# Kernel tuning notes

Measured on AMD Instinct MI355X. Metric: run time of the kernel, lower is better.

## Reference

```python
import jax, jax.numpy as jnp
import numpy as np

MAX_K_QK = 32
MAX_K_V = 32
MAX_K_KNOW = 64
N_HEADS = 12
EPS = 1e-8
LN_EPS = 1e-6


def layer_norm(x, scale, bias):
    mean = jnp.mean(x, axis=-1, keepdims=True)
    var = jnp.mean(jnp.square(x - mean), axis=-1, keepdims=True)
    return (x - mean) / jnp.sqrt(var + LN_EPS) * scale + bias


def threshold_gate(scores, tau, max_k):
    raw = scores - tau
    gate = jnp.where(raw > 0, raw, 1e-8 * jnp.exp(raw))
    exp_gate = jnp.exp(gate) - 1.0
    k = min(max_k, scores.shape[-1])
    topk_vals, _ = jax.lax.top_k(exp_gate, k)
    thr = topk_vals[:, :, -1:]
    exp_gate = jnp.where(exp_gate >= thr, exp_gate, 0.0)
    gate_sum = exp_gate.sum(axis=-1, keepdims=True) + EPS
    gate_strength = jnp.tanh(exp_gate.max(axis=-1, keepdims=True))
    return exp_gate / gate_sum * gate_strength


@jax.checkpoint
def sense_emit_sparse(x, emb, w, gate, idx):
    # x:[B,S,D] emb/w:[N,D] gate/idx:[B,S,k] -> [B,S,D]
    sel_emb = emb[idx]
    sel_w = w[idx]
    act = jnp.einsum('bsd,bskd->bsk', x, sel_emb) * gate
    return jnp.einsum('bsk,bskd->bsd', act, sel_w)


def _forward(x, qk_emb, qk_w, v_emb, v_w, know_emb, know_w, neuron_emb,
             proj_attn_k, proj_attn_b, proj_know_k, proj_know_b,
             tau_attn_k, tau_attn_b, tau_know_k, tau_know_b,
             expand_O, ln1_scale, ln1_bias, ln2_scale, ln2_bias):
    B, S, D = x.shape
    n_qk = qk_emb.shape[0]
    n_v = v_emb.shape[0]
    n_know = know_emb.shape[0]
    emb_norm = neuron_emb / (jnp.linalg.norm(neuron_emb, axis=-1, keepdims=True) + EPS)
    qk_low = emb_norm[:n_qk]
    v_low = emb_norm[n_qk:n_qk + n_v]
    know_low = emb_norm[n_qk + n_v:]

    # ---- attention circuit (deterministic: dropout = identity) ----
    xn = layer_norm(x, ln1_scale, ln1_bias)
    h_all = xn @ proj_attn_k + proj_attn_b
    h_Q, h_K, h_V = jnp.split(h_all, 3, axis=-1)
    tau_all = xn @ tau_attn_k + tau_attn_b
    g_Q = threshold_gate(h_Q @ qk_low.T, tau_all[:, :, 0:1], MAX_K_QK)
    g_K = threshold_gate(h_K @ qk_low.T, tau_all[:, :, 1:2], MAX_K_QK)
    g_V = threshold_gate(h_V @ v_low.T, tau_all[:, :, 2:3], MAX_K_V)
    tk_g_Q, tk_i_Q = jax.lax.top_k(g_Q, MAX_K_QK)
    tk_g_K, tk_i_K = jax.lax.top_k(g_K, MAX_K_QK)
    tk_g_V, tk_i_V = jax.lax.top_k(g_V, MAX_K_V)
    Q = sense_emit_sparse(xn, qk_emb, qk_w, tk_g_Q, tk_i_Q)
    K = sense_emit_sparse(xn, qk_emb, qk_w, tk_g_K, tk_i_K)
    V = sense_emit_sparse(xn, v_emb, v_w, tk_g_V, tk_i_V)
    d_head = D // N_HEADS
    Q = Q.reshape(B, S, N_HEADS, d_head).transpose(0, 2, 1, 3)
    K = K.reshape(B, S, N_HEADS, d_head).transpose(0, 2, 1, 3)
    V = V.reshape(B, S, N_HEADS, d_head).transpose(0, 2, 1, 3)
    scores = jnp.einsum('bhsd,bhtd->bhst', Q, K) / jnp.sqrt(jnp.float32(d_head))
    causal = jnp.tril(jnp.ones((S, S), dtype=jnp.bool_))
    scores = jnp.where(causal, scores, jnp.finfo(scores.dtype).min)
    attn_w = jax.nn.softmax(scores, axis=-1)
    attn_out = jnp.einsum('bhst,bhtd->bhsd', attn_w, V)
    attn_out = attn_out.transpose(0, 2, 1, 3).reshape(B, S, D) @ expand_O
    t_qk, t_v = 1.0 / n_qk, 1.0 / n_v
    a_aux = (((g_Q.mean(axis=(0, 1)) - t_qk) ** 2).sum() * n_qk
             + ((g_K.mean(axis=(0, 1)) - t_qk) ** 2).sum() * n_qk
             + ((g_V.mean(axis=(0, 1)) - t_v) ** 2).sum() * n_v)
    x = x + attn_out

    # ---- knowledge circuit ----
    xn = layer_norm(x, ln2_scale, ln2_bias)
    h = xn @ proj_know_k + proj_know_b
    tau = xn @ tau_know_k + tau_know_b
    gate = threshold_gate(h @ know_low.T, tau, MAX_K_KNOW)
    tk_gate, tk_idx = jax.lax.top_k(gate, MAX_K_KNOW)
    know_out = sense_emit_sparse(xn, know_emb, know_w, tk_gate, tk_idx)
    t_k = 1.0 / n_know
    k_aux = ((gate.mean(axis=(0, 1)) - t_k) ** 2).sum() * n_know
    x = x + know_out
    return x, a_aux + k_aux


def _unit_norm(key, shape):
    v = jax.random.normal(key, shape, jnp.float32)
    return v / (jnp.linalg.norm(v, axis=-1, keepdims=True) + 1e-8)


def setup_inputs() -> dict:
    key = jax.random.key(0)
    ks = jax.random.split(key, 16)
    B, S, D = 4, 1024, 768
    d_space, n_qk, n_v, n_know = 128, 1024, 1024, 4096
    return {
        'x': jax.random.normal(ks[0], (B, S, D), jnp.float32),
        'qk_emb': _unit_norm(ks[1], (n_qk, D)),
        'qk_w': _unit_norm(ks[2], (n_qk, D)),
        'v_emb': _unit_norm(ks[3], (n_v, D)),
        'v_w': _unit_norm(ks[4], (n_v, D)),
        'know_emb': _unit_norm(ks[5], (n_know, D)),
        'know_w': _unit_norm(ks[6], (n_know, D)),
        'neuron_emb': jax.random.normal(ks[7], (n_qk + n_v + n_know, d_space), jnp.float32) * 0.02,
        'proj_attn_k': jax.random.normal(ks[8], (D, 3 * d_space), jnp.float32) * 0.02,
        'proj_attn_b': jnp.zeros((3 * d_space,), jnp.float32),
        'proj_know_k': jax.random.normal(ks[9], (D, d_space), jnp.float32) * 0.02,
        'proj_know_b': jnp.zeros((d_space,), jnp.float32),
        'tau_attn_k': jax.random.normal(ks[10], (D, 3), jnp.float32) * 0.02,
        'tau_attn_b': jnp.zeros((3,), jnp.float32),
        'tau_know_k': jax.random.normal(ks[11], (D, 1), jnp.float32) * 0.02,
        'tau_know_b': jnp.zeros((1,), jnp.float32),
        'expand_O': jax.random.normal(ks[12], (D, D), jnp.float32) * 0.02,
        'ln1_scale': jnp.ones((D,), jnp.float32),
        'ln1_bias': jnp.zeros((D,), jnp.float32),
        'ln2_scale': jnp.ones((D,), jnp.float32),
        'ln2_bias': jnp.zeros((D,), jnp.float32),
    }


def reference(x, qk_emb, qk_w, v_emb, v_w, know_emb, know_w, neuron_emb,
              proj_attn_k, proj_attn_b, proj_know_k, proj_know_b,
              tau_attn_k, tau_attn_b, tau_know_k, tau_know_b,
              expand_O, ln1_scale, ln1_bias, ln2_scale, ln2_bias):
    return _forward(x, qk_emb, qk_w, v_emb, v_w, know_emb, know_w, neuron_emb,
                    proj_attn_k, proj_attn_b, proj_know_k, proj_know_b,
                    tau_attn_k, tau_attn_b, tau_know_k, tau_know_b,
                    expand_O, ln1_scale, ln1_bias, ln2_scale, ln2_bias)
```

## Files before the change

kernel.cpp:

```cpp
#include <hip/hip_runtime.h>
#include <math.h>

#define TOK 4096

#define O_EMBN   0
#define O_XN     786432
#define O_HALL   3932160
#define O_TAU    5505024
#define O_TAUK   5517312
#define O_GVQ    5521408
#define O_GVK    5652480
#define O_GVV    5783552
#define O_GIQ    5914624
#define O_GIK    6045696
#define O_GIV    6176768
#define O_QB     6307840
#define O_KB     9453568
#define O_VB     12599296
#define O_SUM    15745024

__global__ void k_zero(float* p, int n){
  int i = blockIdx.x*blockDim.x + threadIdx.x;
  if (i < n) p[i] = 0.f;
}

__global__ void k_normemb(const float* __restrict__ e, float* __restrict__ o){
  int row = blockIdx.x; int t = threadIdx.x;
  float v = e[(size_t)row*128 + t];
  __shared__ float red[128];
  red[t] = v*v; __syncthreads();
  for (int s=64; s>0; s>>=1){ if (t<s) red[t]+=red[t+s]; __syncthreads(); }
  float norm = sqrtf(red[0]) + 1e-8f;
  o[(size_t)row*128 + t] = v / norm;
}

__global__ void k_ln(const float* __restrict__ x, const float* __restrict__ sc,
                     const float* __restrict__ bi, float* __restrict__ o){
  int tok = blockIdx.x; int t = threadIdx.x;
  __shared__ float red[256];
  const float* xr = x + (size_t)tok*768;
  float a0=xr[t], a1=xr[t+256], a2=xr[t+512];
  red[t] = a0+a1+a2; __syncthreads();
  for (int s=128; s>0; s>>=1){ if (t<s) red[t]+=red[t+s]; __syncthreads(); }
  float mean = red[0] * (1.f/768.f);
  __syncthreads();
  float d0=a0-mean, d1=a1-mean, d2=a2-mean;
  red[t] = d0*d0+d1*d1+d2*d2; __syncthreads();
  for (int s=128; s>0; s>>=1){ if (t<s) red[t]+=red[t+s]; __syncthreads(); }
  float den = sqrtf(red[0]*(1.f/768.f) + 1e-6f);
  float* orow = o + (size_t)tok*768;
  orow[t]     = d0/den*sc[t]     + bi[t];
  orow[t+256] = d1/den*sc[t+256] + bi[t+256];
  orow[t+512] = d2/den*sc[t+512] + bi[t+512];
}

template<bool RES>
__global__ void k_gemm(const float* __restrict__ A, const float* __restrict__ W,
                       const float* __restrict__ bias, const float* __restrict__ res,
                       float* __restrict__ out, int N){
  __shared__ float sA[64][65];
  __shared__ float sW[64][65];
  int t = threadIdx.x;
  int nc0 = blockIdx.x << 6;
  int m0  = blockIdx.y << 6;
  int ty = t >> 4, tx = t & 15;
  float acc[4][4] = {{0.f}};
  for (int kc=0; kc<768; kc+=64){
    __syncthreads();
    #pragma unroll
    for (int i=0;i<4;i++){
      int idx = t + (i<<8); int r = idx>>4, c4=(idx&15)<<2;
      float4 a4 = *(const float4*)(A + (size_t)(m0+r)*768 + kc + c4);
      sA[r][c4]=a4.x; sA[r][c4+1]=a4.y; sA[r][c4+2]=a4.z; sA[r][c4+3]=a4.w;
      float4 w4 = *(const float4*)(W + (size_t)(kc+r)*N + nc0 + c4);
      sW[r][c4]=w4.x; sW[r][c4+1]=w4.y; sW[r][c4+2]=w4.z; sW[r][c4+3]=w4.w;
    }
    __syncthreads();
    #pragma unroll 4
    for (int d=0; d<64; d++){
      float a0=sA[ty*4+0][d], a1=sA[ty*4+1][d], a2=sA[ty*4+2][d], a3=sA[ty*4+3][d];
      float b0=sW[d][tx*4+0], b1=sW[d][tx*4+1], b2=sW[d][tx*4+2], b3=sW[d][tx*4+3];
      acc[0][0]+=a0*b0; acc[0][1]+=a0*b1; acc[0][2]+=a0*b2; acc[0][3]+=a0*b3;
      acc[1][0]+=a1*b0; acc[1][1]+=a1*b1; acc[1][2]+=a1*b2; acc[1][3]+=a1*b3;
      acc[2][0]+=a2*b0; acc[2][1]+=a2*b1; acc[2][2]+=a2*b2; acc[2][3]+=a2*b3;
      acc[3][0]+=a3*b0; acc[3][1]+=a3*b1; acc[3][2]+=a3*b2; acc[3][3]+=a3*b3;
    }
  }
  #pragma unroll
  for (int i=0;i<4;i++){
    int row = m0 + ty*4 + i;
    #pragma unroll
    for (int j=0;j<4;j++){
      int col = nc0 + tx*4 + j;
      float v = acc[i][j];
      if (bias) v += bias[col];
      if (RES)  v += res[(size_t)row*768 + col];
      out[(size_t)row*N + col] = v;
    }
  }
}

__global__ void k_tau(const float* __restrict__ xn, const float* __restrict__ tW,
                      const float* __restrict__ tb, float* __restrict__ tout, int tc){
  int tok = blockIdx.x;
  int t = threadIdx.x;
  int col = t >> 6, lane = t & 63;
  const float* xr = xn + (size_t)tok*768;
  float v = 0.f;
  for (int d=lane; d<768; d+=64) v += xr[d]*tW[(size_t)d*tc + col];
  #pragma unroll
  for (int off=32; off; off>>=1) v += __shfl_down(v, off);
  if (lane==0) tout[(size_t)tok*tc + col] = v + tb[col];
}

__global__ void k_score(const float* __restrict__ h, int hstride, int hoff,
                        const float* __restrict__ taub, int tstride, int toff,
                        const float* __restrict__ low,
                        float* __restrict__ outg, int n, int tok0){
  __shared__ float sh[64][129];
  __shared__ float sl[64][129];
  __shared__ float stau[64];
  int t = threadIdx.x;
  int nrow0 = blockIdx.x << 6;
  int trow0 = blockIdx.y << 6;
  #pragma unroll
  for (int k=0;k<8;k++){
    int idx = t + (k<<8);
    int r = idx >> 5, c4 = (idx & 31) << 2;
    const float* src = h + (size_t)(tok0 + trow0 + r)*hstride + hoff + c4;
    float4 x4 = *(const float4*)src;
    sh[r][c4]=x4.x; sh[r][c4+1]=x4.y; sh[r][c4+2]=x4.z; sh[r][c4+3]=x4.w;
    const float* src2 = low + (size_t)(nrow0 + r)*128 + c4;
    float4 y4 = *(const float4*)src2;
    sl[r][c4]=y4.x; sl[r][c4+1]=y4.y; sl[r][c4+2]=y4.z; sl[r][c4+3]=y4.w;
  }
  if (t < 64) stau[t] = taub[(size_t)(tok0 + trow0 + t)*tstride + toff];
  __syncthreads();
  int ty = t >> 4, tx = t & 15;
  float acc[4][4] = {{0.f}};
  #pragma unroll 4
  for (int d=0; d<128; d++){
    float a0=sh[ty*4+0][d], a1=sh[ty*4+1][d], a2=sh[ty*4+2][d], a3=sh[ty*4+3][d];
    float b0=sl[tx*4+0][d], b1=sl[tx*4+1][d], b2=sl[tx*4+2][d], b3=sl[tx*4+3][d];
    acc[0][0]+=a0*b0; acc[0][1]+=a0*b1; acc[0][2]+=a0*b2; acc[0][3]+=a0*b3;
    acc[1][0]+=a1*b0; acc[1][1]+=a1*b1; acc[1][2]+=a1*b2; acc[1][3]+=a1*b3;
    acc[2][0]+=a2*b0; acc[2][1]+=a2*b1; acc[2][2]+=a2*b2; acc[2][3]+=a2*b3;
    acc[3][0]+=a3*b0; acc[3][1]+=a3*b1; acc[3][2]+=a3*b2; acc[3][3]+=a3*b3;
  }
  #pragma unroll
  for (int i=0;i<4;i++){
    int tt = trow0 + ty*4 + i;
    float tau = stau[ty*4+i];
    #pragma unroll
    for (int j=0;j<4;j++){
      float raw = acc[i][j] - tau;
      float g = raw > 0.f ? raw : 1e-8f*expf(raw);
      outg[(size_t)tt*n + nrow0 + tx*4 + j] = expf(g) - 1.0f;
    }
  }
}

template<int ITEMS, int K>
__global__ void k_select(const float* __restrict__ sc, int n, int tok0,
                         float* __restrict__ gval, int* __restrict__ gidx,
                         float* __restrict__ sums){
  int tl = blockIdx.x; int t = threadIdx.x;
  float v[ITEMS];
  const float* row = sc + (size_t)tl*n;
  #pragma unroll
  for (int i=0;i<ITEMS;i++) v[i] = row[t + (i<<8)];
  __shared__ float wv[4]; __shared__ int wi[4];
  __shared__ float s0; __shared__ float stot;
  float myval = 0.f; int myidx = 0;
  int w = t >> 6, lane = t & 63;
  for (int it=0; it<K; it++){
    float mv = v[0]; int mi = t;
    #pragma unroll
    for (int i=1;i<ITEMS;i++){
      float vi = v[i];
      if (vi > mv){ mv = vi; mi = t + (i<<8); }
    }
    #pragma unroll
    for (int off=32; off; off>>=1){
      float ov = __shfl_xor(mv, off);
      int   oi = __shfl_xor(mi, off);
      if (ov > mv || (ov == mv && oi < mi)){ mv = ov; mi = oi; }
    }
    if (lane==0){ wv[w]=mv; wi[w]=mi; }
    __syncthreads();
    float bv = wv[0]; int bi = wi[0];
    #pragma unroll
    for (int k=1;k<4;k++){
      float ov=wv[k]; int oi=wi[k];
      if (ov > bv || (ov == bv && oi < bi)){ bv=ov; bi=oi; }
    }
    if (t == (bi & 255)){
      #pragma unroll
      for (int i=0;i<ITEMS;i++) if (i == (bi >> 8)) v[i] = -1.f;
    }
    if (t == it){ myval = bv; myidx = bi; }
    if (it==0 && t==0) s0 = tanhf(bv);
    __syncthreads();
  }
  float c = (t < K) ? myval : 0.f;
  #pragma unroll
  for (int off=32; off; off>>=1) c += __shfl_xor(c, off);
  if (lane==0) wv[w]=c;
  __syncthreads();
  if (t==0) stot = wv[0]+wv[1]+wv[2]+wv[3] + 1e-8f;
  __syncthreads();
  if (t < K){
    float nv = myval / stot * s0;
    size_t o = (size_t)(tok0 + tl)*K + t;
    gval[o] = nv; gidx[o] = myidx;
    atomicAdd(&sums[myidx], nv);
  }
}

__global__ void k_sense(const float* __restrict__ xn, const float* __restrict__ emb,
                        const float* __restrict__ w, const float* __restrict__ gval,
                        const int* __restrict__ gidx, float* __restrict__ out,
                        int K, int acc){
  int tok = blockIdx.x; int t = threadIdx.x;
  __shared__ float sxn[768]; __shared__ float sact[64]; __shared__ int sidx[64];
  const float* xr = xn + (size_t)tok*768;
  for (int d=t; d<768; d+=256) sxn[d]=xr[d];
  if (t < K) sidx[t] = gidx[(size_t)tok*K + t];
  __syncthreads();
  int tpk = 256 / K;
  int k = t / tpk, p = t % tpk;
  const float* er = emb + (size_t)sidx[k]*768;
  float v = 0.f;
  for (int d=p; d<768; d+=tpk) v += sxn[d]*er[d];
  for (int off=tpk>>1; off; off>>=1) v += __shfl_down(v, off);
  if (p==0) sact[k] = v * gval[(size_t)tok*K + k];
  __syncthreads();
  float* orow = out + (size_t)tok*768;
  for (int d=t; d<768; d+=256){
    float o = 0.f;
    for (int kk=0; kk<K; kk++) o += sact[kk]*w[(size_t)sidx[kk]*768 + d];
    if (acc) orow[d] += o; else orow[d] = o;
  }
}

__global__ void k_attn(const float* __restrict__ Q, const float* __restrict__ K,
                       const float* __restrict__ V, float* __restrict__ ao){
  __shared__ float sQ[64][65];
  __shared__ float sKV[64][65];
  __shared__ float sP[64][65];
  int qt = gridDim.x - 1 - blockIdx.x;
  int h = blockIdx.y, b = blockIdx.z;
  int t = threadIdx.x;
  int ty = t >> 4, tx = t & 15;
  size_t base = ((size_t)b*1024)*768 + (size_t)h*64;
  int q0 = qt << 6;
  #pragma unroll
  for (int i=0;i<4;i++){
    int idx = t + (i<<8); int r = idx>>4, c4 = (idx&15)<<2;
    float4 v4 = *(const float4*)(Q + base + (size_t)(q0+r)*768 + c4);
    sQ[r][c4]=v4.x; sQ[r][c4+1]=v4.y; sQ[r][c4+2]=v4.z; sQ[r][c4+3]=v4.w;
  }
  float m[4], l[4], o[4][4];
  #pragma unroll
  for (int r=0;r<4;r++){
    m[r] = -INFINITY; l[r] = 0.f;
    #pragma unroll
    for (int c=0;c<4;c++) o[r][c] = 0.f;
  }
  for (int kt=0; kt<=qt; kt++){
    int t0 = kt << 6;
    __syncthreads();
    #pragma unroll
    for (int i=0;i<4;i++){
      int idx = t + (i<<8); int r = idx>>4, c4=(idx&15)<<2;
      float4 kv = *(const float4*)(K + base + (size_t)(t0+r)*768 + c4);
      sKV[r][c4]=kv.x; sKV[r][c4+1]=kv.y; sKV[r][c4+2]=kv.z; sKV[r][c4+3]=kv.w;
    }
    __syncthreads();
    float s[4][4] = {{0.f}};
    #pragma unroll 4
    for (int d=0; d<64; d++){
      float a0=sQ[ty*4+0][d], a1=sQ[ty*4+1][d], a2=sQ[ty*4+2][d], a3=sQ[ty*4+3][d];
      float b0=sKV[tx*4+0][d], b1=sKV[tx*4+1][d], b2=sKV[tx*4+2][d], b3=sKV[tx*4+3][d];
      s[0][0]+=a0*b0; s[0][1]+=a0*b1; s[0][2]+=a0*b2; s[0][3]+=a0*b3;
      s[1][0]+=a1*b0; s[1][1]+=a1*b1; s[1][2]+=a1*b2; s[1][3]+=a1*b3;
      s[2][0]+=a2*b0; s[2][1]+=a2*b1; s[2][2]+=a2*b2; s[2][3]+=a2*b3;
      s[3][0]+=a3*b0; s[3][1]+=a3*b1; s[3][2]+=a3*b2; s[3][3]+=a3*b3;
    }
    bool diag = (kt == qt);
    #pragma unroll
    for (int r=0;r<4;r++){
      #pragma unroll
      for (int c=0;c<4;c++){
        s[r][c] *= 0.125f;
        if (diag && (tx*4+c > ty*4+r)) s[r][c] = -INFINITY;
      }
    }
    float scl[4];
    #pragma unroll
    for (int r=0;r<4;r++){
      float tm = fmaxf(fmaxf(s[r][0],s[r][1]), fmaxf(s[r][2],s[r][3]));
      #pragma unroll
      for (int off=8; off; off>>=1) tm = fmaxf(tm, __shfl_xor(tm, off));
      float mn = fmaxf(m[r], tm);
      float sc = expf(m[r] - mn);
      float ps = 0.f;
      #pragma unroll
      for (int c=0;c<4;c++){
        float p = expf(s[r][c] - mn);
        s[r][c] = p; ps += p;
        sP[ty*4+r][tx*4+c] = p;
      }
      #pragma unroll
      for (int off=8; off; off>>=1) ps += __shfl_xor(ps, off);
      l[r] = l[r]*sc + ps;
      m[r] = mn;
      scl[r] = sc;
    }
    #pragma unroll
    for (int r=0;r<4;r++){
      #pragma unroll
      for (int c=0;c<4;c++) o[r][c] *= scl[r];
    }
    __syncthreads();
    #pragma unroll
    for (int i=0;i<4;i++){
      int idx = t + (i<<8); int r = idx>>4, c4=(idx&15)<<2;
      float4 vv = *(const float4*)(V + base + (size_t)(t0+r)*768 + c4);
      sKV[r][c4]=vv.x; sKV[r][c4+1]=vv.y; sKV[r][c4+2]=vv.z; sKV[r][c4+3]=vv.w;
    }
    __syncthreads();
    #pragma unroll 4
    for (int k=0;k<64;k++){
      float p0=sP[ty*4+0][k], p1=sP[ty*4+1][k], p2=sP[ty*4+2][k], p3=sP[ty*4+3][k];
      float v0=sKV[k][tx*4+0], v1=sKV[k][tx*4+1], v2=sKV[k][tx*4+2], v3=sKV[k][tx*4+3];
      o[0][0]+=p0*v0; o[0][1]+=p0*v1; o[0][2]+=p0*v2; o[0][3]+=p0*v3;
      o[1][0]+=p1*v0; o[1][1]+=p1*v1; o[1][2]+=p1*v2; o[1][3]+=p1*v3;
      o[2][0]+=p2*v0; o[2][1]+=p2*v1; o[2][2]+=p2*v2; o[2][3]+=p2*v3;
      o[3][0]+=p3*v0; o[3][1]+=p3*v1; o[3][2]+=p3*v2; o[3][3]+=p3*v3;
    }
  }
  #pragma unroll
  for (int r=0;r<4;r++){
    float inv = 1.f / l[r];
    #pragma unroll
    for (int c=0;c<4;c++)
      ao[base + (size_t)(q0+ty*4+r)*768 + tx*4+c] = o[r][c]*inv;
  }
}

__global__ void k_aux(const float* __restrict__ sums, float* __restrict__ out){
  int t = threadIdx.x;
  __shared__ float red[256];
  float a = 0.f;
  const float inv = 1.f/4096.f;
  const float tq = 1.f/1024.f;
  for (int j=t; j<1024; j+=256){
    float d0 = sums[j]*inv        - tq; a += d0*d0*1024.f;
    float d1 = sums[1024+j]*inv   - tq; a += d1*d1*1024.f;
    float d2 = sums[2048+j]*inv   - tq; a += d2*d2*1024.f;
  }
  const float tk = 1.f/4096.f;
  for (int j=t; j<4096; j+=256){
    float d3 = sums[3072+j]*inv - tk; a += d3*d3*4096.f;
  }
  red[t]=a; __syncthreads();
  for (int s=128; s>0; s>>=1){ if (t<s) red[t]+=red[t+s]; __syncthreads(); }
  if (t==0) out[0] = red[0];
}

extern "C" void kernel_launch(void* const* d_in, const int* in_sizes, int n_in,
                              void* d_out, int out_size, void* d_ws, size_t ws_size,
                              hipStream_t stream){
  const float* x        = (const float*)d_in[0];
  const float* qk_emb   = (const float*)d_in[1];
  const float* qk_w     = (const float*)d_in[2];
  const float* v_emb    = (const float*)d_in[3];
  const float* v_w      = (const float*)d_in[4];
  const float* know_emb = (const float*)d_in[5];
  const float* know_w   = (const float*)d_in[6];
  const float* neuron_emb = (const float*)d_in[7];
  const float* pak  = (const float*)d_in[8];
  const float* pab  = (const float*)d_in[9];
  const float* pkk  = (const float*)d_in[10];
  const float* pkb  = (const float*)d_in[11];
  const float* tak  = (const float*)d_in[12];
  const float* tab  = (const float*)d_in[13];
  const float* tkk  = (const float*)d_in[14];
  const float* tkb  = (const float*)d_in[15];
  const float* expO = (const float*)d_in[16];
  const float* ln1s = (const float*)d_in[17];
  const float* ln1b = (const float*)d_in[18];
  const float* ln2s = (const float*)d_in[19];
  const float* ln2b = (const float*)d_in[20];
  float* out = (float*)d_out;
  float* ws  = (float*)d_ws;

  k_zero<<<28,256,0,stream>>>(ws+O_SUM, 7168);
  k_normemb<<<6144,128,0,stream>>>(neuron_emb, ws+O_EMBN);
  k_ln<<<4096,256,0,stream>>>(x, ln1s, ln1b, ws+O_XN);
  k_gemm<false><<<dim3(6,64),256,0,stream>>>(ws+O_XN, pak, pab, nullptr, ws+O_HALL, 384);
  k_tau<<<4096,192,0,stream>>>(ws+O_XN, tak, tab, ws+O_TAU, 3);

  float* sc = ws + O_QB;
  k_score<<<dim3(16,64),256,0,stream>>>(ws+O_HALL,384,0,   ws+O_TAU,3,0, ws+O_EMBN, sc, 1024, 0);
  k_select<4,32><<<4096,256,0,stream>>>(sc, 1024, 0, ws+O_GVQ,(int*)(ws+O_GIQ), ws+O_SUM);
  k_score<<<dim3(16,64),256,0,stream>>>(ws+O_HALL,384,128, ws+O_TAU,3,1, ws+O_EMBN, sc, 1024, 0);
  k_select<4,32><<<4096,256,0,stream>>>(sc, 1024, 0, ws+O_GVK,(int*)(ws+O_GIK), ws+O_SUM+1024);
  k_score<<<dim3(16,64),256,0,stream>>>(ws+O_HALL,384,256, ws+O_TAU,3,2, ws+O_EMBN+1024*128, sc, 1024, 0);
  k_select<4,32><<<4096,256,0,stream>>>(sc, 1024, 0, ws+O_GVV,(int*)(ws+O_GIV), ws+O_SUM+2048);

  k_sense<<<4096,256,0,stream>>>(ws+O_XN, qk_emb, qk_w, ws+O_GVQ,(int*)(ws+O_GIQ), ws+O_QB, 32,0);
  k_sense<<<4096,256,0,stream>>>(ws+O_XN, qk_emb, qk_w, ws+O_GVK,(int*)(ws+O_GIK), ws+O_KB, 32,0);
  k_sense<<<4096,256,0,stream>>>(ws+O_XN, v_emb,  v_w,  ws+O_GVV,(int*)(ws+O_GIV), ws+O_VB, 32,0);

  k_attn<<<dim3(16,12,4),256,0,stream>>>(ws+O_QB, ws+O_KB, ws+O_VB, ws+O_XN);

  k_gemm<true><<<dim3(12,64),256,0,stream>>>(ws+O_XN, expO, nullptr, x, out, 768);

  k_ln<<<4096,256,0,stream>>>(out, ln2s, ln2b, ws+O_QB);
  k_gemm<false><<<dim3(2,64),256,0,stream>>>(ws+O_QB, pkk, pkb, nullptr, ws+O_HALL, 128);
  k_tau<<<4096,64,0,stream>>>(ws+O_QB, tkk, tkb, ws+O_TAUK, 1);

  float* sck = ws + O_KB;
  for (int c=0; c<4; c++){
    int tok0 = c*1024;
    k_score<<<dim3(64,16),256,0,stream>>>(ws+O_HALL,128,0, ws+O_TAUK,1,0, ws+O_EMBN+2048*128, sck, 4096, tok0);
    k_select<16,64><<<1024,256,0,stream>>>(sck, 4096, tok0, ws+O_GVQ,(int*)(ws+O_GIQ), ws+O_SUM+3072);
  }

  k_sense<<<4096,256,0,stream>>>(ws+O_QB, know_emb, know_w, ws+O_GVQ,(int*)(ws+O_GIQ), out, 64,1);

  k_aux<<<1,256,0,stream>>>(ws+O_SUM, out + 3145728);
}
```

Measured before the change: 2.065 ms.

## Vectorize shared-memory tiles, register-prefetch K/V, and rebalance causal attention scheduling

Rewrites the GEMM, score and attention inner loops to use float4 shared-memory stores and loads with padded [64][68] tiles, and switches to a strided column mapping (tx+16*j) to cut LDS instruction count and bank conflicts. The score kernel now runs its 128-wide reduction as two 64-wide chunks so shared memory shrinks. The attention kernel prefetches the next K/V tile into registers while computing the current one, loads V together with K into a separate buffer, and reuses the K buffer for P. It also permutes query-tile assignment across blocks to balance causal work. Adds launch bounds; register pressure from the prefetch registers could lower occupancy.

```diff
diff --git a/kernel.cpp b/kernel.cpp
--- a/kernel.cpp
+++ b/kernel.cpp
@@ -55,11 +55,11 @@
 }
 
 template<bool RES>
-__global__ void k_gemm(const float* __restrict__ A, const float* __restrict__ W,
+__global__ __launch_bounds__(256) void k_gemm(const float* __restrict__ A, const float* __restrict__ W,
                        const float* __restrict__ bias, const float* __restrict__ res,
                        float* __restrict__ out, int N){
-  __shared__ float sA[64][65];
-  __shared__ float sW[64][65];
+  __shared__ float sA[64][68];
+  __shared__ float sW[64][68];
   int t = threadIdx.x;
   int nc0 = blockIdx.x << 6;
   int m0  = blockIdx.y << 6;
@@ -70,29 +70,36 @@
     #pragma unroll
     for (int i=0;i<4;i++){
       int idx = t + (i<<8); int r = idx>>4, c4=(idx&15)<<2;
-      float4 a4 = *(const float4*)(A + (size_t)(m0+r)*768 + kc + c4);
-      sA[r][c4]=a4.x; sA[r][c4+1]=a4.y; sA[r][c4+2]=a4.z; sA[r][c4+3]=a4.w;
-      float4 w4 = *(const float4*)(W + (size_t)(kc+r)*N + nc0 + c4);
-      sW[r][c4]=w4.x; sW[r][c4+1]=w4.y; sW[r][c4+2]=w4.z; sW[r][c4+3]=w4.w;
-    }
-    __syncthreads();
-    #pragma unroll 4
-    for (int d=0; d<64; d++){
-      float a0=sA[ty*4+0][d], a1=sA[ty*4+1][d], a2=sA[ty*4+2][d], a3=sA[ty*4+3][d];
-      float b0=sW[d][tx*4+0], b1=sW[d][tx*4+1], b2=sW[d][tx*4+2], b3=sW[d][tx*4+3];
-      acc[0][0]+=a0*b0; acc[0][1]+=a0*b1; acc[0][2]+=a0*b2; acc[0][3]+=a0*b3;
-      acc[1][0]+=a1*b0; acc[1][1]+=a1*b1; acc[1][2]+=a1*b2; acc[1][3]+=a1*b3;
-      acc[2][0]+=a2*b0; acc[2][1]+=a2*b1; acc[2][2]+=a2*b2; acc[2][3]+=a2*b3;
-      acc[3][0]+=a3*b0; acc[3][1]+=a3*b1; acc[3][2]+=a3*b2; acc[3][3]+=a3*b3;
-    }
-  }
-  #pragma unroll
-  for (int i=0;i<4;i++){
-    int row = m0 + ty*4 + i;
+      *(float4*)&sA[r][c4] = *(const float4*)(A + (size_t)(m0+r)*768 + kc + c4);
+      *(float4*)&sW[r][c4] = *(const float4*)(W + (size_t)(kc+r)*N + nc0 + c4);
+    }
+    __syncthreads();
+    #pragma unroll 2
+    for (int d4=0; d4<64; d4+=4){
+      float aa[4][4];
+      #pragma unroll
+      for (int r=0;r<4;r++){
+        float4 a4 = *(const float4*)&sA[ty*4+r][d4];
+        aa[r][0]=a4.x; aa[r][1]=a4.y; aa[r][2]=a4.z; aa[r][3]=a4.w;
+      }
+      #pragma unroll
+      for (int dd=0; dd<4; dd++){
+        float w0=sW[d4+dd][tx], w1=sW[d4+dd][tx+16], w2=sW[d4+dd][tx+32], w3=sW[d4+dd][tx+48];
+        #pragma unroll
+        for (int r=0;r<4;r++){
+          acc[r][0]+=aa[r][dd]*w0; acc[r][1]+=aa[r][dd]*w1;
+          acc[r][2]+=aa[r][dd]*w2; acc[r][3]+=aa[r][dd]*w3;
+        }
+      }
+    }
+  }
+  #pragma unroll
+  for (int r=0;r<4;r++){
+    int row = m0 + ty*4 + r;
     #pragma unroll
     for (int j=0;j<4;j++){
-      int col = nc0 + tx*4 + j;
-      float v = acc[i][j];
+      int col = nc0 + tx + 16*j;
+      float v = acc[r][j];
       if (bias) v += bias[col];
       if (RES)  v += res[(size_t)row*768 + col];
       out[(size_t)row*N + col] = v;
@@ -113,39 +120,43 @@
   if (lane==0) tout[(size_t)tok*tc + col] = v + tb[col];
 }
 
-__global__ void k_score(const float* __restrict__ h, int hstride, int hoff,
+__global__ __launch_bounds__(256) void k_score(const float* __restrict__ h, int hstride, int hoff,
                         const float* __restrict__ taub, int tstride, int toff,
                         const float* __restrict__ low,
                         float* __restrict__ outg, int n, int tok0){
-  __shared__ float sh[64][129];
-  __shared__ float sl[64][129];
+  __shared__ float sh[64][68];
+  __shared__ float sl[64][68];
   __shared__ float stau[64];
   int t = threadIdx.x;
   int nrow0 = blockIdx.x << 6;
   int trow0 = blockIdx.y << 6;
-  #pragma unroll
-  for (int k=0;k<8;k++){
-    int idx = t + (k<<8);
-    int r = idx >> 5, c4 = (idx & 31) << 2;
-    const float* src = h + (size_t)(tok0 + trow0 + r)*hstride + hoff + c4;
-    float4 x4 = *(const float4*)src;
-    sh[r][c4]=x4.x; sh[r][c4+1]=x4.y; sh[r][c4+2]=x4.z; sh[r][c4+3]=x4.w;
-    const float* src2 = low + (size_t)(nrow0 + r)*128 + c4;
-    float4 y4 = *(const float4*)src2;
-    sl[r][c4]=y4.x; sl[r][c4+1]=y4.y; sl[r][c4+2]=y4.z; sl[r][c4+3]=y4.w;
-  }
+  int ty = t >> 4, tx = t & 15;
   if (t < 64) stau[t] = taub[(size_t)(tok0 + trow0 + t)*tstride + toff];
-  __syncthreads();
-  int ty = t >> 4, tx = t & 15;
   float acc[4][4] = {{0.f}};
-  #pragma unroll 4
-  for (int d=0; d<128; d++){
-    float a0=sh[ty*4+0][d], a1=sh[ty*4+1][d], a2=sh[ty*4+2][d], a3=sh[ty*4+3][d];
-    float b0=sl[tx*4+0][d], b1=sl[tx*4+1][d], b2=sl[tx*4+2][d], b3=sl[tx*4+3][d];
-    acc[0][0]+=a0*b0; acc[0][1]+=a0*b1; acc[0][2]+=a0*b2; acc[0][3]+=a0*b3;
-    acc[1][0]+=a1*b0; acc[1][1]+=a1*b1; acc[1][2]+=a1*b2; acc[1][3]+=a1*b3;
-    acc[2][0]+=a2*b0; acc[2][1]+=a2*b1; acc[2][2]+=a2*b2; acc[2][3]+=a2*b3;
-    acc[3][0]+=a3*b0; acc[3][1]+=a3*b1; acc[3][2]+=a3*b2; acc[3][3]+=a3*b3;
+  for (int kc=0; kc<128; kc+=64){
+    __syncthreads();
+    #pragma unroll
+    for (int i=0;i<4;i++){
+      int idx = t + (i<<8); int r = idx>>4, c4=(idx&15)<<2;
+      *(float4*)&sh[r][c4] = *(const float4*)(h + (size_t)(tok0+trow0+r)*hstride + hoff + kc + c4);
+      *(float4*)&sl[r][c4] = *(const float4*)(low + (size_t)(nrow0+r)*128 + kc + c4);
+    }
+    __syncthreads();
+    #pragma unroll 2
+    for (int d4=0; d4<64; d4+=4){
+      float4 ha[4], lb[4];
+      #pragma unroll
+      for (int r=0;r<4;r++) ha[r] = *(const float4*)&sh[ty*4+r][d4];
+      #pragma unroll
+      for (int j=0;j<4;j++) lb[j] = *(const float4*)&sl[tx+16*j][d4];
+      #pragma unroll
+      for (int r=0;r<4;r++){
+        #pragma unroll
+        for (int j=0;j<4;j++){
+          acc[r][j] += ha[r].x*lb[j].x + ha[r].y*lb[j].y + ha[r].z*lb[j].z + ha[r].w*lb[j].w;
+        }
+      }
+    }
   }
   #pragma unroll
   for (int i=0;i<4;i++){
@@ -155,7 +166,7 @@
     for (int j=0;j<4;j++){
       float raw = acc[i][j] - tau;
       float g = raw > 0.f ? raw : 1e-8f*expf(raw);
-      outg[(size_t)tt*n + nrow0 + tx*4 + j] = expf(g) - 1.0f;
+      outg[(size_t)tt*n + nrow0 + tx + 16*j] = expf(g) - 1.0f;
     }
   }
 }
@@ -224,7 +235,7 @@
   int tok = blockIdx.x; int t = threadIdx.x;
   __shared__ float sxn[768]; __shared__ float sact[64]; __shared__ int sidx[64];
   const float* xr = xn + (size_t)tok*768;
-  for (int d=t; d<768; d+=256) sxn[d]=xr[d];
+  if (t < 192) *(float4*)&sxn[t*4] = *(const float4*)(xr + t*4);
   if (t < K) sidx[t] = gidx[(size_t)tok*K + t];
   __syncthreads();
   int tpk = 256 / K;
@@ -243,12 +254,13 @@
   }
 }
 
-__global__ void k_attn(const float* __restrict__ Q, const float* __restrict__ K,
+__global__ __launch_bounds__(256) void k_attn(const float* __restrict__ Q, const float* __restrict__ K,
                        const float* __restrict__ V, float* __restrict__ ao){
-  __shared__ float sQ[64][65];
-  __shared__ float sKV[64][65];
-  __shared__ float sP[64][65];
-  int qt = gridDim.x - 1 - blockIdx.x;
+  __shared__ float sQ[64][68];
+  __shared__ float sKP[64][68];
+  __shared__ float sV[64][68];
+  int flat = blockIdx.x + (blockIdx.y<<4) + blockIdx.z*192;
+  int qt = (blockIdx.x + 5*(flat>>8)) & 15;
   int h = blockIdx.y, b = blockIdx.z;
   int t = threadIdx.x;
   int ty = t >> 4, tx = t & 15;
@@ -257,46 +269,66 @@
   #pragma unroll
   for (int i=0;i<4;i++){
     int idx = t + (i<<8); int r = idx>>4, c4 = (idx&15)<<2;
-    float4 v4 = *(const float4*)(Q + base + (size_t)(q0+r)*768 + c4);
-    sQ[r][c4]=v4.x; sQ[r][c4+1]=v4.y; sQ[r][c4+2]=v4.z; sQ[r][c4+3]=v4.w;
+    *(float4*)&sQ[r][c4] = *(const float4*)(Q + base + (size_t)(q0+r)*768 + c4);
+  }
+  float4 kreg[4], vreg[4];
+  #pragma unroll
+  for (int i=0;i<4;i++){
+    int idx = t + (i<<8); int r = idx>>4, c4=(idx&15)<<2;
+    kreg[i] = *(const float4*)(K + base + (size_t)r*768 + c4);
+    vreg[i] = *(const float4*)(V + base + (size_t)r*768 + c4);
   }
   float m[4], l[4], o[4][4];
   #pragma unroll
   for (int r=0;r<4;r++){
     m[r] = -INFINITY; l[r] = 0.f;
     #pragma unroll
-    for (int c=0;c<4;c++) o[r][c] = 0.f;
+    for (int j=0;j<4;j++) o[r][j] = 0.f;
   }
   for (int kt=0; kt<=qt; kt++){
-    int t0 = kt << 6;
     __syncthreads();
     #pragma unroll
     for (int i=0;i<4;i++){
       int idx = t + (i<<8); int r = idx>>4, c4=(idx&15)<<2;
-      float4 kv = *(const float4*)(K + base + (size_t)(t0+r)*768 + c4);
-      sKV[r][c4]=kv.x; sKV[r][c4+1]=kv.y; sKV[r][c4+2]=kv.z; sKV[r][c4+3]=kv.w;
+      *(float4*)&sKP[r][c4] = kreg[i];
+      *(float4*)&sV[r][c4]  = vreg[i];
+    }
+    if (kt < qt){
+      int t0n = (kt+1) << 6;
+      #pragma unroll
+      for (int i=0;i<4;i++){
+        int idx = t + (i<<8); int r = idx>>4, c4=(idx&15)<<2;
+        kreg[i] = *(const float4*)(K + base + (size_t)(t0n+r)*768 + c4);
+        vreg[i] = *(const float4*)(V + base + (size_t)(t0n+r)*768 + c4);
+      }
     }
     __syncthreads();
     float s[4][4] = {{0.f}};
-    #pragma unroll 4
-    for (int d=0; d<64; d++){
-      float a0=sQ[ty*4+0][d], a1=sQ[ty*4+1][d], a2=sQ[ty*4+2][d], a3=sQ[ty*4+3][d];
-      float b0=sKV[tx*4+0][d], b1=sKV[tx*4+1][d], b2=sKV[tx*4+2][d], b3=sKV[tx*4+3][d];
-      s[0][0]+=a0*b0; s[0][1]+=a0*b1; s[0][2]+=a0*b2; s[0][3]+=a0*b3;
-      s[1][0]+=a1*b0; s[1][1]+=a1*b1; s[1][2]+=a1*b2; s[1][3]+=a1*b3;
-      s[2][0]+=a2*b0; s[2][1]+=a2*b1; s[2][2]+=a2*b2; s[2][3]+=a2*b3;
-      s[3][0]+=a3*b0; s[3][1]+=a3*b1; s[3][2]+=a3*b2; s[3][3]+=a3*b3;
+    #pragma unroll 2
+    for (int d4=0; d4<64; d4+=4){
+      float4 qa[4], kb[4];
+      #pragma unroll
+      for (int r=0;r<4;r++) qa[r] = *(const float4*)&sQ[ty*4+r][d4];
+      #pragma unroll
+      for (int j=0;j<4;j++) kb[j] = *(const float4*)&sKP[tx+16*j][d4];
+      #pragma unroll
+      for (int r=0;r<4;r++){
+        #pragma unroll
+        for (int j=0;j<4;j++){
+          s[r][j] += qa[r].x*kb[j].x + qa[r].y*kb[j].y + qa[r].z*kb[j].z + qa[r].w*kb[j].w;
+        }
+      }
     }
     bool diag = (kt == qt);
     #pragma unroll
     for (int r=0;r<4;r++){
-      #pragma unroll
-      for (int c=0;c<4;c++){
-        s[r][c] *= 0.125f;
-        if (diag && (tx*4+c > ty*4+r)) s[r][c] = -INFINITY;
-      }
-    }
-    float scl[4];
+      int row = ty*4+r;
+      #pragma unroll
+      for (int j=0;j<4;j++){
+        s[r][j] *= 0.125f;
+        if (diag && (tx+16*j > row)) s[r][j] = -INFINITY;
+      }
+    }
     #pragma unroll
     for (int r=0;r<4;r++){
       float tm = fmaxf(fmaxf(s[r][0],s[r][1]), fmaxf(s[r][2],s[r][3]));
@@ -306,46 +338,49 @@
       float sc = expf(m[r] - mn);
       float ps = 0.f;
       #pragma unroll
-      for (int c=0;c<4;c++){
-        float p = expf(s[r][c] - mn);
-        s[r][c] = p; ps += p;
-        sP[ty*4+r][tx*4+c] = p;
+      for (int j=0;j<4;j++){
+        float p = expf(s[r][j] - mn);
+        s[r][j] = p; ps += p;
       }
       #pragma unroll
       for (int off=8; off; off>>=1) ps += __shfl_xor(ps, off);
       l[r] = l[r]*sc + ps;
       m[r] = mn;
-      scl[r] = sc;
-    }
+      #pragma unroll
+      for (int j=0;j<4;j++) o[r][j] *= sc;
+    }
+    __syncthreads();
     #pragma unroll
     for (int r=0;r<4;r++){
       #pragma unroll
-      for (int c=0;c<4;c++) o[r][c] *= scl[r];
-    }
-    __syncthreads();
-    #pragma unroll
-    for (int i=0;i<4;i++){
-      int idx = t + (i<<8); int r = idx>>4, c4=(idx&15)<<2;
-      float4 vv = *(const float4*)(V + base + (size_t)(t0+r)*768 + c4);
-      sKV[r][c4]=vv.x; sKV[r][c4+1]=vv.y; sKV[r][c4+2]=vv.z; sKV[r][c4+3]=vv.w;
-    }
-    __syncthreads();
-    #pragma unroll 4
-    for (int k=0;k<64;k++){
-      float p0=sP[ty*4+0][k], p1=sP[ty*4+1][k], p2=sP[ty*4+2][k], p3=sP[ty*4+3][k];
-      float v0=sKV[k][tx*4+0], v1=sKV[k][tx*4+1], v2=sKV[k][tx*4+2], v3=sKV[k][tx*4+3];
-      o[0][0]+=p0*v0; o[0][1]+=p0*v1; o[0][2]+=p0*v2; o[0][3]+=p0*v3;
-      o[1][0]+=p1*v0; o[1][1]+=p1*v1; o[1][2]+=p1*v2; o[1][3]+=p1*v3;
-      o[2][0]+=p2*v0; o[2][1]+=p2*v1; o[2][2]+=p2*v2; o[2][3]+=p2*v3;
-      o[3][0]+=p3*v0; o[3][1]+=p3*v1; o[3][2]+=p3*v2; o[3][3]+=p3*v3;
+      for (int j=0;j<4;j++) sKP[ty*4+r][tx+16*j] = s[r][j];
+    }
+    __syncthreads();
+    #pragma unroll 2
+    for (int k4=0; k4<64; k4+=4){
+      float pas[4][4];
+      #pragma unroll
+      for (int r=0;r<4;r++){
+        float4 tp = *(const float4*)&sKP[ty*4+r][k4];
+        pas[r][0]=tp.x; pas[r][1]=tp.y; pas[r][2]=tp.z; pas[r][3]=tp.w;
+      }
+      #pragma unroll
+      for (int kk=0; kk<4; kk++){
+        float v0=sV[k4+kk][tx], v1=sV[k4+kk][tx+16], v2=sV[k4+kk][tx+32], v3=sV[k4+kk][tx+48];
+        #pragma unroll
+        for (int r=0;r<4;r++){
+          o[r][0]+=pas[r][kk]*v0; o[r][1]+=pas[r][kk]*v1;
+          o[r][2]+=pas[r][kk]*v2; o[r][3]+=pas[r][kk]*v3;
+        }
+      }
     }
   }
   #pragma unroll
   for (int r=0;r<4;r++){
     float inv = 1.f / l[r];
     #pragma unroll
-    for (int c=0;c<4;c++)
-      ao[base + (size_t)(q0+ty*4+r)*768 + tx*4+c] = o[r][c]*inv;
+    for (int j=0;j<4;j++)
+      ao[base + (size_t)(q0+ty*4+r)*768 + tx + 16*j] = o[r][j]*inv;
   }
 }
 
```

Measured after the change: 1.855 ms. 10.1% less time.
